# Optimization experiments

Hardware: AMD Instinct MI355X
Metric: run time of the kernel (lower is better)

The kernel has to match this reference:

```python
import jax, jax.numpy as jnp
import numpy as np

T, B, D_IN, H = 512, 64, 512, 1024


def setup_inputs() -> dict:
    key = jax.random.key(0)
    ks = jax.random.split(key, 6)
    s = 1.0 / np.sqrt(D_IN + H)  # torch Linear default init scale
    return {
        "x": jax.random.normal(ks[0], (T, B, D_IN), jnp.float32),
        "h0": jnp.zeros((B, H), jnp.float32),
        "C0": jnp.zeros((B, H), jnp.float32),
        "W_in": jax.random.normal(ks[1], (D_IN + H, H), jnp.float32) * s,
        "b_in": jnp.zeros((H,), jnp.float32),
        "W_over": jax.random.normal(ks[2], (D_IN + H, H), jnp.float32) * s,
        "b_over": jnp.zeros((H,), jnp.float32),
        "W_out": jax.random.normal(ks[3], (D_IN + H, H), jnp.float32) * s,
        "b_out": jnp.zeros((H,), jnp.float32),
        "W_intern": jax.random.normal(ks[4], (D_IN + H, H), jnp.float32) * s,
        "b_intern": jnp.zeros((H,), jnp.float32),
    }


def reference(x, h0, C0, W_in, b_in, W_over, b_over, W_out, b_out, W_intern, b_intern):
    # Faithful translation: concat order is (h, x) per one_step.
    def step(carry, xt):
        h, C = carry
        xc = jnp.concatenate([h, xt], axis=1)               # [B, H + D_IN]
        to_keep = jax.nn.sigmoid(xc @ W_in + b_in)          # input gate
        to_throw = jax.nn.sigmoid(xc @ W_over + b_over)     # forget gate
        out = jax.nn.sigmoid(xc @ W_out + b_out)            # output gate
        Ct = to_throw * C + to_keep * jnp.tanh(xc @ W_intern + b_intern)
        ht = out * jnp.tanh(Ct)
        return (ht, Ct), ht

    (hT, CT), hs = jax.lax.scan(step, (h0, C0), x)
    return hs, CT  # ([T, B, H], [B, H])
```

## Files before the change

### kernel.cpp

```cpp
#include <hip/hip_runtime.h>
#include <hip/hip_bf16.h>
#include <stdint.h>

#define T_STEPS 512
#define BATCH   64
#define DIN     512
#define HID     1024
#define KDIM    1536
#define NBLK    128
#define HPB     8
#define GCPB    32
#define KGRPS   192

typedef __bf16 bf16x8 __attribute__((ext_vector_type(8)));
typedef float  f32x4  __attribute__((ext_vector_type(4)));
typedef unsigned short ushort_t;
typedef unsigned long long u64_t;

__device__ __forceinline__ ushort_t f2bf(float f) {
    union { float f; unsigned u; } v; v.f = f;
    unsigned u = v.u;
    u += 0x7FFFu + ((u >> 16) & 1u);
    return (ushort_t)(u >> 16);
}

__device__ __forceinline__ float fast_sig(float x) {
    return __builtin_amdgcn_rcpf(1.0f + __expf(-x));
}
__device__ __forceinline__ float fast_tanh(float x) {
    float e = __expf(2.0f * x);
    return 1.0f - 2.0f * __builtin_amdgcn_rcpf(e + 1.0f);
}

__global__ void cvt_x(const float* __restrict__ x, ushort_t* __restrict__ xb, int n8) {
    int i = blockIdx.x * blockDim.x + threadIdx.x;
    if (i >= n8) return;
    float4 v0 = ((const float4*)x)[2 * i];
    float4 v1 = ((const float4*)x)[2 * i + 1];
    uint4 o;
    o.x = (unsigned)f2bf(v0.x) | ((unsigned)f2bf(v0.y) << 16);
    o.y = (unsigned)f2bf(v0.z) | ((unsigned)f2bf(v0.w) << 16);
    o.z = (unsigned)f2bf(v1.x) | ((unsigned)f2bf(v1.y) << 16);
    o.w = (unsigned)f2bf(v1.z) | ((unsigned)f2bf(v1.w) << 16);
    ((uint4*)xb)[i] = o;
}

__global__ void xpose_w(const float* __restrict__ Wi, const float* __restrict__ Wf,
                        const float* __restrict__ Wo, const float* __restrict__ Wg,
                        ushort_t* __restrict__ wt) {
    __shared__ float tile[64][65];
    int kt = blockIdx.x, nt = blockIdx.y, g = blockIdx.z;
    const float* W = (g == 0) ? Wi : (g == 1) ? Wf : (g == 2) ? Wo : Wg;
    int k0 = kt * 64, n0 = nt * 64;
    int c = threadIdx.x & 63, r0 = threadIdx.x >> 6;
#pragma unroll
    for (int i = 0; i < 16; ++i) {
        int r = r0 + i * 4;
        tile[r][c] = W[(size_t)(k0 + r) * HID + n0 + c];
    }
    __syncthreads();
#pragma unroll
    for (int p = 0; p < 2; ++p) {
        int q = threadIdx.x + p * 256;
        int n_inner = q & 7;
        int kgl = (q >> 3) & 7;
        int bl = q >> 6;
        int n = n0 + bl * 8 + n_inner;
        int blk = n >> 3;
        int nn = g * 8 + (n & 7);
        int kgrp = (k0 >> 3) + kgl;
        __align__(16) ushort_t tmp[8];
#pragma unroll
        for (int j = 0; j < 8; ++j) tmp[j] = f2bf(tile[kgl * 8 + j][bl * 8 + n_inner]);
        *(uint4*)(wt + ((((size_t)blk * KGRPS + kgrp) * GCPB + nn) << 3)) = *(const uint4*)tmp;
    }
}

__global__ __launch_bounds__(256, 1) void lstm_persist(
    const ushort_t* __restrict__ xbf,
    const ushort_t* __restrict__ wt,
    const float* __restrict__ h0, const float* __restrict__ C0,
    const float* __restrict__ b_i, const float* __restrict__ b_f,
    const float* __restrict__ b_o, const float* __restrict__ b_g,
    ushort_t* __restrict__ hbuf,
    unsigned* __restrict__ flags,
    float* __restrict__ out)
{
    __shared__ __align__(16) ushort_t Wl[KGRPS][GCPB + 1][8];
    __shared__ float gbuf[4][BATCH][GCPB + 1];
    __shared__ float Cl[BATCH][HPB + 1];
    __shared__ float biasl[GCPB];

    const int tid  = threadIdx.x;
    const int blk  = blockIdx.x;
    const int wave = tid >> 6;
    const int lane = tid & 63;
    const int j0   = blk * HPB;

    {
        const uint4* src = (const uint4*)(wt + (size_t)blk * KGRPS * GCPB * 8);
        uint4* dst = (uint4*)(&Wl[0][0][0]);
        for (int i = tid; i < 6144; i += 256) {
            int kgrp = i >> 5, n = i & 31;
            dst[kgrp * (GCPB + 1) + n] = src[i];
        }
    }
    if (tid < GCPB) {
        int g = tid >> 3, j = tid & 7;
        const float* bp = (g == 0) ? b_i : (g == 1) ? b_f : (g == 2) ? b_o : b_g;
        biasl[tid] = bp[j0 + j];
    }
    if (tid < 128) {
        int b = tid >> 1, jh = (tid & 1) * 4;
#pragma unroll
        for (int jj = 0; jj < 4; ++jj)
            Cl[b][jh + jj] = C0[b * HID + j0 + jh + jj];
        u64_t pk = 0;
#pragma unroll
        for (int jj = 0; jj < 4; ++jj)
            pk |= (u64_t)f2bf(h0[b * HID + j0 + jh + jj]) << (16 * jj);
        __hip_atomic_store((u64_t*)(hbuf + b * HID + j0 + jh), pk,
                           __ATOMIC_RELAXED, __HIP_MEMORY_SCOPE_AGENT);
    }
    asm volatile("s_waitcnt vmcnt(0)" ::: "memory");
    __syncthreads();
    if (tid == 0)
        __hip_atomic_store(&flags[blk * 32], 1u, __ATOMIC_RELAXED, __HIP_MEMORY_SCOPE_AGENT);

    const int m_lane = lane & 15;
    const int quad   = lane >> 4;
    const int koff   = quad * 8;
    int pb = 0;

    for (int t = 0; t < T_STEPS; ++t) {
        const ushort_t* hsrc = hbuf + pb * BATCH * HID;
        const ushort_t* xsrc = xbf + (size_t)t * BATCH * DIN;

        f32x4 acc[4][2];
#pragma unroll
        for (int rt = 0; rt < 4; ++rt)
#pragma unroll
            for (int ct = 0; ct < 2; ++ct)
                acc[rt][ct] = (f32x4){0.f, 0.f, 0.f, 0.f};

#pragma unroll
        for (int cc = 0; cc < 4; ++cc) {
            const int c = 32 + wave * 4 + cc;
            const ushort_t* ap = xsrc + (c - 32) * 32 + koff;
            bf16x8 a[4];
#pragma unroll
            for (int rt = 0; rt < 4; ++rt)
                a[rt] = *(const bf16x8*)(ap + (size_t)(rt * 16 + m_lane) * DIN);
            const int kgrp = c * 4 + quad;
            bf16x8 b0 = *(const bf16x8*)(&Wl[kgrp][m_lane][0]);
            bf16x8 b1 = *(const bf16x8*)(&Wl[kgrp][16 + m_lane][0]);
#pragma unroll
            for (int rt = 0; rt < 4; ++rt) {
                acc[rt][0] = __builtin_amdgcn_mfma_f32_16x16x32_bf16(a[rt], b0, acc[rt][0], 0, 0, 0);
                acc[rt][1] = __builtin_amdgcn_mfma_f32_16x16x32_bf16(a[rt], b1, acc[rt][1], 0, 0, 0);
            }
        }

        if (tid < NBLK) {
            while (__hip_atomic_load(&flags[tid * 32], __ATOMIC_RELAXED,
                                     __HIP_MEMORY_SCOPE_AGENT) < (unsigned)(t + 1))
                __builtin_amdgcn_s_sleep(1);
        }
        __syncthreads();
        __builtin_amdgcn_fence(__ATOMIC_ACQUIRE, "agent");

        bf16x8 ah[8][4];
#pragma unroll
        for (int cc = 0; cc < 8; ++cc) {
            const ushort_t* ap = hsrc + (wave * 8 + cc) * 32 + koff;
#pragma unroll
            for (int rt = 0; rt < 4; ++rt)
                ah[cc][rt] = *(const bf16x8*)(ap + (size_t)(rt * 16 + m_lane) * HID);
        }
        __builtin_amdgcn_sched_barrier(0);

#pragma unroll
        for (int cc = 0; cc < 8; ++cc) {
            const int kgrp = (wave * 8 + cc) * 4 + quad;
            bf16x8 b0 = *(const bf16x8*)(&Wl[kgrp][m_lane][0]);
            bf16x8 b1 = *(const bf16x8*)(&Wl[kgrp][16 + m_lane][0]);
#pragma unroll
            for (int rt = 0; rt < 4; ++rt) {
                acc[rt][0] = __builtin_amdgcn_mfma_f32_16x16x32_bf16(ah[cc][rt], b0, acc[rt][0], 0, 0, 0);
                acc[rt][1] = __builtin_amdgcn_mfma_f32_16x16x32_bf16(ah[cc][rt], b1, acc[rt][1], 0, 0, 0);
            }
        }

#pragma unroll
        for (int rt = 0; rt < 4; ++rt)
#pragma unroll
            for (int ct = 0; ct < 2; ++ct)
#pragma unroll
                for (int r = 0; r < 4; ++r)
                    gbuf[wave][rt * 16 + quad * 4 + r][ct * 16 + m_lane] = acc[rt][ct][r];
        __syncthreads();

        float hv[4], cv[4];
        int b = tid >> 1, jh = (tid & 1) * 4;
        if (tid < 128) {
#pragma unroll
            for (int jj = 0; jj < 4; ++jj) {
                int j = jh + jj;
                float pre[4];
#pragma unroll
                for (int g = 0; g < 4; ++g) {
                    int col = g * 8 + j;
                    pre[g] = biasl[col] + gbuf[0][b][col] + gbuf[1][b][col]
                                        + gbuf[2][b][col] + gbuf[3][b][col];
                }
                float ig = fast_sig(pre[0]);
                float fg = fast_sig(pre[1]);
                float og = fast_sig(pre[2]);
                float gg = fast_tanh(pre[3]);
                float c_new = fg * Cl[b][jh + jj] + ig * gg;
                Cl[b][jh + jj] = c_new;
                cv[jj] = c_new;
                hv[jj] = og * fast_tanh(c_new);
            }
            u64_t pk = (u64_t)f2bf(hv[0]) | ((u64_t)f2bf(hv[1]) << 16)
                     | ((u64_t)f2bf(hv[2]) << 32) | ((u64_t)f2bf(hv[3]) << 48);
            __hip_atomic_store((u64_t*)(hbuf + (1 - pb) * BATCH * HID + b * HID + j0 + jh),
                               pk, __ATOMIC_RELAXED, __HIP_MEMORY_SCOPE_AGENT);
        }
        asm volatile("s_waitcnt vmcnt(0)" ::: "memory");
        __syncthreads();
        if (tid == 0)
            __hip_atomic_store(&flags[blk * 32], (unsigned)(t + 2), __ATOMIC_RELAXED,
                               __HIP_MEMORY_SCOPE_AGENT);

        if (tid < 128) {
            float4 o4; o4.x = hv[0]; o4.y = hv[1]; o4.z = hv[2]; o4.w = hv[3];
            *(float4*)(out + (size_t)t * BATCH * HID + b * HID + j0 + jh) = o4;
            if (t == T_STEPS - 1) {
                float4 c4; c4.x = cv[0]; c4.y = cv[1]; c4.z = cv[2]; c4.w = cv[3];
                *(float4*)(out + (size_t)T_STEPS * BATCH * HID + b * HID + j0 + jh) = c4;
            }
        }
        pb ^= 1;
    }
}

extern "C" void kernel_launch(void* const* d_in, const int* in_sizes, int n_in,
                              void* d_out, int out_size, void* d_ws, size_t ws_size,
                              hipStream_t stream) {
    (void)in_sizes; (void)n_in; (void)out_size; (void)ws_size;
    const float* x  = (const float*)d_in[0];
    const float* h0 = (const float*)d_in[1];
    const float* C0 = (const float*)d_in[2];
    const float* Wi = (const float*)d_in[3];
    const float* bi = (const float*)d_in[4];
    const float* Wf = (const float*)d_in[5];
    const float* bf = (const float*)d_in[6];
    const float* Wo = (const float*)d_in[7];
    const float* bo = (const float*)d_in[8];
    const float* Wg = (const float*)d_in[9];
    const float* bg = (const float*)d_in[10];
    float* out = (float*)d_out;

    char* ws = (char*)d_ws;
    unsigned*  flags = (unsigned*)ws;
    ushort_t*  hbuf  = (ushort_t*)(ws + 16384);
    ushort_t*  xb    = (ushort_t*)(ws + 16384 + 262144);
    ushort_t*  wt    = (ushort_t*)(ws + 16384 + 262144 + 33554432);

    hipMemsetAsync(flags, 0, 16384, stream);
    cvt_x<<<8192, 256, 0, stream>>>(x, xb, (T_STEPS * BATCH * DIN) / 8);
    xpose_w<<<dim3(24, 16, 4), 256, 0, stream>>>(Wi, Wf, Wo, Wg, wt);
    lstm_persist<<<NBLK, 256, 0, stream>>>(xb, wt, h0, C0, bi, bf, bo, bg, hbuf, flags, out);
}
```

Baseline: 5.169 ms.

## Keep per-block weights in registers and defer x-projection MFMAs past barrier

Each wave now holds its slice of the weight tile (x and h parts) in VGPRs for the whole kernel instead of staging the tile in LDS and re-reading it every step. The x-input loads are issued before the inter-block flag wait, but their MFMAs now run after it, together with the h MFMAs. Empty asm statements force the loaded operands to be live before the MFMAs. This drops per-step LDS weight traffic at the cost of much higher register pressure (24 bf16x8 weight vectors plus 48 activation vectors per lane), which risks spills. The x-projection compute also moves onto the critical path after the sync instead of overlapping with the wait. The gbuf row pad changes from 33 to 34 floats.

```diff
diff --git a/kernel.cpp b/kernel.cpp
--- a/kernel.cpp
+++ b/kernel.cpp
@@ -86,8 +86,7 @@
     unsigned* __restrict__ flags,
     float* __restrict__ out)
 {
-    __shared__ __align__(16) ushort_t Wl[KGRPS][GCPB + 1][8];
-    __shared__ float gbuf[4][BATCH][GCPB + 1];
+    __shared__ float gbuf[4][BATCH][GCPB + 2];
     __shared__ float Cl[BATCH][HPB + 1];
     __shared__ float biasl[GCPB];
 
@@ -96,15 +95,25 @@
     const int wave = tid >> 6;
     const int lane = tid & 63;
     const int j0   = blk * HPB;
-
-    {
-        const uint4* src = (const uint4*)(wt + (size_t)blk * KGRPS * GCPB * 8);
-        uint4* dst = (uint4*)(&Wl[0][0][0]);
-        for (int i = tid; i < 6144; i += 256) {
-            int kgrp = i >> 5, n = i & 31;
-            dst[kgrp * (GCPB + 1) + n] = src[i];
-        }
-    }
+    const int m_lane = lane & 15;
+    const int quad   = lane >> 4;
+    const int koff   = quad * 8;
+
+    const ushort_t* wblk = wt + (size_t)blk * KGRPS * GCPB * 8;
+    bf16x8 wbx[4][2], wbh[8][2];
+#pragma unroll
+    for (int cc = 0; cc < 4; ++cc) {
+        const int kgrp = (32 + wave * 4 + cc) * 4 + quad;
+        wbx[cc][0] = *(const bf16x8*)(wblk + ((size_t)kgrp * GCPB + m_lane) * 8);
+        wbx[cc][1] = *(const bf16x8*)(wblk + ((size_t)kgrp * GCPB + 16 + m_lane) * 8);
+    }
+#pragma unroll
+    for (int cc = 0; cc < 8; ++cc) {
+        const int kgrp = (wave * 8 + cc) * 4 + quad;
+        wbh[cc][0] = *(const bf16x8*)(wblk + ((size_t)kgrp * GCPB + m_lane) * 8);
+        wbh[cc][1] = *(const bf16x8*)(wblk + ((size_t)kgrp * GCPB + 16 + m_lane) * 8);
+    }
+
     if (tid < GCPB) {
         int g = tid >> 3, j = tid & 7;
         const float* bp = (g == 0) ? b_i : (g == 1) ? b_f : (g == 2) ? b_o : b_g;
@@ -127,14 +136,10 @@
     if (tid == 0)
         __hip_atomic_store(&flags[blk * 32], 1u, __ATOMIC_RELAXED, __HIP_MEMORY_SCOPE_AGENT);
 
-    const int m_lane = lane & 15;
-    const int quad   = lane >> 4;
-    const int koff   = quad * 8;
     int pb = 0;
-
     for (int t = 0; t < T_STEPS; ++t) {
+        const ushort_t* xsrc = xbf + (size_t)t * BATCH * DIN;
         const ushort_t* hsrc = hbuf + pb * BATCH * HID;
-        const ushort_t* xsrc = xbf + (size_t)t * BATCH * DIN;
 
         f32x4 acc[4][2];
 #pragma unroll
@@ -143,23 +148,15 @@
             for (int ct = 0; ct < 2; ++ct)
                 acc[rt][ct] = (f32x4){0.f, 0.f, 0.f, 0.f};
 
+        bf16x8 ax[4][4];
 #pragma unroll
         for (int cc = 0; cc < 4; ++cc) {
-            const int c = 32 + wave * 4 + cc;
-            const ushort_t* ap = xsrc + (c - 32) * 32 + koff;
-            bf16x8 a[4];
+            const ushort_t* ap = xsrc + (wave * 4 + cc) * 32 + koff;
 #pragma unroll
             for (int rt = 0; rt < 4; ++rt)
-                a[rt] = *(const bf16x8*)(ap + (size_t)(rt * 16 + m_lane) * DIN);
-            const int kgrp = c * 4 + quad;
-            bf16x8 b0 = *(const bf16x8*)(&Wl[kgrp][m_lane][0]);
-            bf16x8 b1 = *(const bf16x8*)(&Wl[kgrp][16 + m_lane][0]);
-#pragma unroll
-            for (int rt = 0; rt < 4; ++rt) {
-                acc[rt][0] = __builtin_amdgcn_mfma_f32_16x16x32_bf16(a[rt], b0, acc[rt][0], 0, 0, 0);
-                acc[rt][1] = __builtin_amdgcn_mfma_f32_16x16x32_bf16(a[rt], b1, acc[rt][1], 0, 0, 0);
-            }
-        }
+                ax[cc][rt] = *(const bf16x8*)(ap + (size_t)(rt * 16 + m_lane) * DIN);
+        }
+        __builtin_amdgcn_sched_barrier(0);
 
         if (tid < NBLK) {
             while (__hip_atomic_load(&flags[tid * 32], __ATOMIC_RELAXED,
@@ -179,17 +176,37 @@
         }
         __builtin_amdgcn_sched_barrier(0);
 
-#pragma unroll
-        for (int cc = 0; cc < 8; ++cc) {
-            const int kgrp = (wave * 8 + cc) * 4 + quad;
-            bf16x8 b0 = *(const bf16x8*)(&Wl[kgrp][m_lane][0]);
-            bf16x8 b1 = *(const bf16x8*)(&Wl[kgrp][16 + m_lane][0]);
+        asm volatile("" ::
+            "v"(ax[0][0]), "v"(ax[0][1]), "v"(ax[0][2]), "v"(ax[0][3]),
+            "v"(ax[1][0]), "v"(ax[1][1]), "v"(ax[1][2]), "v"(ax[1][3]),
+            "v"(ax[2][0]), "v"(ax[2][1]), "v"(ax[2][2]), "v"(ax[2][3]),
+            "v"(ax[3][0]), "v"(ax[3][1]), "v"(ax[3][2]), "v"(ax[3][3]));
+#pragma unroll
+        for (int cc = 0; cc < 4; ++cc)
 #pragma unroll
             for (int rt = 0; rt < 4; ++rt) {
-                acc[rt][0] = __builtin_amdgcn_mfma_f32_16x16x32_bf16(ah[cc][rt], b0, acc[rt][0], 0, 0, 0);
-                acc[rt][1] = __builtin_amdgcn_mfma_f32_16x16x32_bf16(ah[cc][rt], b1, acc[rt][1], 0, 0, 0);
-            }
-        }
+                acc[rt][0] = __builtin_amdgcn_mfma_f32_16x16x32_bf16(ax[cc][rt], wbx[cc][0], acc[rt][0], 0, 0, 0);
+                acc[rt][1] = __builtin_amdgcn_mfma_f32_16x16x32_bf16(ax[cc][rt], wbx[cc][1], acc[rt][1], 0, 0, 0);
+            }
+
+        asm volatile("" ::
+            "v"(ah[0][0]), "v"(ah[0][1]), "v"(ah[0][2]), "v"(ah[0][3]),
+            "v"(ah[1][0]), "v"(ah[1][1]), "v"(ah[1][2]), "v"(ah[1][3]),
+            "v"(ah[2][0]), "v"(ah[2][1]), "v"(ah[2][2]), "v"(ah[2][3]),
+            "v"(ah[3][0]), "v"(ah[3][1]), "v"(ah[3][2]), "v"(ah[3][3]));
+        asm volatile("" ::
+            "v"(ah[4][0]), "v"(ah[4][1]), "v"(ah[4][2]), "v"(ah[4][3]),
+            "v"(ah[5][0]), "v"(ah[5][1]), "v"(ah[5][2]), "v"(ah[5][3]),
+            "v"(ah[6][0]), "v"(ah[6][1]), "v"(ah[6][2]), "v"(ah[6][3]),
+            "v"(ah[7][0]), "v"(ah[7][1]), "v"(ah[7][2]), "v"(ah[7][3]));
+
+#pragma unroll
+        for (int cc = 0; cc < 8; ++cc)
+#pragma unroll
+            for (int rt = 0; rt < 4; ++rt) {
+                acc[rt][0] = __builtin_amdgcn_mfma_f32_16x16x32_bf16(ah[cc][rt], wbh[cc][0], acc[rt][0], 0, 0, 0);
+                acc[rt][1] = __builtin_amdgcn_mfma_f32_16x16x32_bf16(ah[cc][rt], wbh[cc][1], acc[rt][1], 0, 0, 0);
+            }
 
 #pragma unroll
         for (int rt = 0; rt < 4; ++rt)
```

New measurement: 5.381 ms. 1.04x slower.

## Warp-specialize LSTM step: recurrent waves with register weights, input waves prefetch x

Applied to the files above, without the earlier changes.

Waves are split into two roles. Waves 0-1 keep the recurrent-weight slice in registers and do only the h·W_h product, the gate math and the h publication. Waves 2-3 keep the input-weight slice in shared memory, compute the x·W_x product, prefetch the next timestep's x, and write the fp32 outputs staged through new shared buffers. The aim is to take the x product, the x loads and the output stores off the serial dependency on the previous step's h, and to drop the recurrent-weight reads from shared memory. In exchange, each recurrent wave now does twice as many h chunks, and register pressure rises sharply.

```diff
diff --git a/kernel.cpp b/kernel.cpp
--- a/kernel.cpp
+++ b/kernel.cpp
@@ -11,6 +11,7 @@
 #define HPB     8
 #define GCPB    32
 #define KGRPS   192
+#define XKG     64
 
 typedef __bf16 bf16x8 __attribute__((ext_vector_type(8)));
 typedef float  f32x4  __attribute__((ext_vector_type(4)));
@@ -86,9 +87,11 @@
     unsigned* __restrict__ flags,
     float* __restrict__ out)
 {
-    __shared__ __align__(16) ushort_t Wl[KGRPS][GCPB + 1][8];
-    __shared__ float gbuf[4][BATCH][GCPB + 1];
+    __shared__ __align__(16) ushort_t Wlx[XKG][GCPB][8];
+    __shared__ float gbuf[4][BATCH][GCPB + 2];
     __shared__ float Cl[BATCH][HPB + 1];
+    __shared__ float hvbuf[BATCH][HPB];
+    __shared__ float cvbuf[BATCH][HPB];
     __shared__ float biasl[GCPB];
 
     const int tid  = threadIdx.x;
@@ -96,15 +99,27 @@
     const int wave = tid >> 6;
     const int lane = tid & 63;
     const int j0   = blk * HPB;
-
+    const int m_lane = lane & 15;
+    const int quad   = lane >> 4;
+    const int koff   = quad * 8;
+
+    const ushort_t* wblk = wt + (size_t)blk * KGRPS * GCPB * 8;
+
+    bf16x8 wbh[16][2];
+    if (wave < 2) {
+#pragma unroll
+        for (int cc = 0; cc < 16; ++cc) {
+            const int kgrp = (wave * 16 + cc) * 4 + quad;
+            wbh[cc][0] = *(const bf16x8*)(wblk + ((size_t)kgrp * GCPB + m_lane) * 8);
+            wbh[cc][1] = *(const bf16x8*)(wblk + ((size_t)kgrp * GCPB + 16 + m_lane) * 8);
+        }
+    }
     {
-        const uint4* src = (const uint4*)(wt + (size_t)blk * KGRPS * GCPB * 8);
-        uint4* dst = (uint4*)(&Wl[0][0][0]);
-        for (int i = tid; i < 6144; i += 256) {
-            int kgrp = i >> 5, n = i & 31;
-            dst[kgrp * (GCPB + 1) + n] = src[i];
-        }
-    }
+        const uint4* src = (const uint4*)(wblk + (size_t)128 * GCPB * 8);
+        uint4* dst = (uint4*)(&Wlx[0][0][0]);
+        for (int i = tid; i < XKG * GCPB; i += 256) dst[i] = src[i];
+    }
+
     if (tid < GCPB) {
         int g = tid >> 3, j = tid & 7;
         const float* bp = (g == 0) ? b_i : (g == 1) ? b_f : (g == 2) ? b_o : b_g;
@@ -127,82 +142,75 @@
     if (tid == 0)
         __hip_atomic_store(&flags[blk * 32], 1u, __ATOMIC_RELAXED, __HIP_MEMORY_SCOPE_AGENT);
 
-    const int m_lane = lane & 15;
-    const int quad   = lane >> 4;
-    const int koff   = quad * 8;
+    bf16x8 ax[8][4];
+    if (wave >= 2) {
+#pragma unroll
+        for (int cc = 0; cc < 8; ++cc) {
+            const ushort_t* ap = xbf + ((wave - 2) * 8 + cc) * 32 + koff;
+#pragma unroll
+            for (int rt = 0; rt < 4; ++rt)
+                ax[cc][rt] = *(const bf16x8*)(ap + (size_t)(rt * 16 + m_lane) * DIN);
+        }
+    }
+
     int pb = 0;
-
     for (int t = 0; t < T_STEPS; ++t) {
-        const ushort_t* hsrc = hbuf + pb * BATCH * HID;
-        const ushort_t* xsrc = xbf + (size_t)t * BATCH * DIN;
-
-        f32x4 acc[4][2];
-#pragma unroll
-        for (int rt = 0; rt < 4; ++rt)
-#pragma unroll
-            for (int ct = 0; ct < 2; ++ct)
-                acc[rt][ct] = (f32x4){0.f, 0.f, 0.f, 0.f};
-
-#pragma unroll
-        for (int cc = 0; cc < 4; ++cc) {
-            const int c = 32 + wave * 4 + cc;
-            const ushort_t* ap = xsrc + (c - 32) * 32 + koff;
-            bf16x8 a[4];
-#pragma unroll
-            for (int rt = 0; rt < 4; ++rt)
-                a[rt] = *(const bf16x8*)(ap + (size_t)(rt * 16 + m_lane) * DIN);
-            const int kgrp = c * 4 + quad;
-            bf16x8 b0 = *(const bf16x8*)(&Wl[kgrp][m_lane][0]);
-            bf16x8 b1 = *(const bf16x8*)(&Wl[kgrp][16 + m_lane][0]);
-#pragma unroll
-            for (int rt = 0; rt < 4; ++rt) {
-                acc[rt][0] = __builtin_amdgcn_mfma_f32_16x16x32_bf16(a[rt], b0, acc[rt][0], 0, 0, 0);
-                acc[rt][1] = __builtin_amdgcn_mfma_f32_16x16x32_bf16(a[rt], b1, acc[rt][1], 0, 0, 0);
-            }
-        }
-
-        if (tid < NBLK) {
+        if (wave < 2) {
             while (__hip_atomic_load(&flags[tid * 32], __ATOMIC_RELAXED,
                                      __HIP_MEMORY_SCOPE_AGENT) < (unsigned)(t + 1))
                 __builtin_amdgcn_s_sleep(1);
-        }
-        __syncthreads();
-        __builtin_amdgcn_fence(__ATOMIC_ACQUIRE, "agent");
-
-        bf16x8 ah[8][4];
-#pragma unroll
-        for (int cc = 0; cc < 8; ++cc) {
-            const ushort_t* ap = hsrc + (wave * 8 + cc) * 32 + koff;
+            __syncthreads();
+            __builtin_amdgcn_fence(__ATOMIC_ACQUIRE, "agent");
+            __builtin_amdgcn_sched_barrier(0);
+
+            const ushort_t* hsrc = hbuf + pb * BATCH * HID;
+            const int hc0 = wave * 16;
+
+            f32x4 acc[4][2];
+#pragma unroll
+            for (int rt = 0; rt < 4; ++rt) {
+                acc[rt][0] = (f32x4){0.f, 0.f, 0.f, 0.f};
+                acc[rt][1] = (f32x4){0.f, 0.f, 0.f, 0.f};
+            }
+
+            bf16x8 a0[4][4], a1[4][4], a2[4][4], a3[4][4];
+#define LOADB(dst, c0)                                                        \
+            _Pragma("unroll") for (int q = 0; q < 4; ++q) {                   \
+                const ushort_t* ap = hsrc + (size_t)(hc0 + (c0) + q) * 32 + koff; \
+                _Pragma("unroll") for (int rt = 0; rt < 4; ++rt)              \
+                    dst[q][rt] = *(const bf16x8*)(ap + (size_t)(rt * 16 + m_lane) * HID); \
+            }
+#define MFMAB(src, c0)                                                        \
+            _Pragma("unroll") for (int q = 0; q < 4; ++q) {                   \
+                _Pragma("unroll") for (int rt = 0; rt < 4; ++rt) {            \
+                    acc[rt][0] = __builtin_amdgcn_mfma_f32_16x16x32_bf16(     \
+                        src[q][rt], wbh[(c0) + q][0], acc[rt][0], 0, 0, 0);   \
+                    acc[rt][1] = __builtin_amdgcn_mfma_f32_16x16x32_bf16(     \
+                        src[q][rt], wbh[(c0) + q][1], acc[rt][1], 0, 0, 0);   \
+                }                                                             \
+            }
+            LOADB(a0, 0)
+            LOADB(a1, 4)
+            MFMAB(a0, 0)
+            LOADB(a2, 8)
+            MFMAB(a1, 4)
+            LOADB(a3, 12)
+            MFMAB(a2, 8)
+            MFMAB(a3, 12)
+#undef LOADB
+#undef MFMAB
+
 #pragma unroll
             for (int rt = 0; rt < 4; ++rt)
-                ah[cc][rt] = *(const bf16x8*)(ap + (size_t)(rt * 16 + m_lane) * HID);
-        }
-        __builtin_amdgcn_sched_barrier(0);
-
-#pragma unroll
-        for (int cc = 0; cc < 8; ++cc) {
-            const int kgrp = (wave * 8 + cc) * 4 + quad;
-            bf16x8 b0 = *(const bf16x8*)(&Wl[kgrp][m_lane][0]);
-            bf16x8 b1 = *(const bf16x8*)(&Wl[kgrp][16 + m_lane][0]);
-#pragma unroll
-            for (int rt = 0; rt < 4; ++rt) {
-                acc[rt][0] = __builtin_amdgcn_mfma_f32_16x16x32_bf16(ah[cc][rt], b0, acc[rt][0], 0, 0, 0);
-                acc[rt][1] = __builtin_amdgcn_mfma_f32_16x16x32_bf16(ah[cc][rt], b1, acc[rt][1], 0, 0, 0);
-            }
-        }
-
-#pragma unroll
-        for (int rt = 0; rt < 4; ++rt)
-#pragma unroll
-            for (int ct = 0; ct < 2; ++ct)
-#pragma unroll
-                for (int r = 0; r < 4; ++r)
-                    gbuf[wave][rt * 16 + quad * 4 + r][ct * 16 + m_lane] = acc[rt][ct][r];
-        __syncthreads();
-
-        float hv[4], cv[4];
-        int b = tid >> 1, jh = (tid & 1) * 4;
-        if (tid < 128) {
+#pragma unroll
+                for (int ct = 0; ct < 2; ++ct)
+#pragma unroll
+                    for (int r = 0; r < 4; ++r)
+                        gbuf[wave][rt * 16 + quad * 4 + r][ct * 16 + m_lane] = acc[rt][ct][r];
+            __syncthreads();
+
+            float hv[4], cv[4];
+            const int b = tid >> 1, jh = (tid & 1) * 4;
 #pragma unroll
             for (int jj = 0; jj < 4; ++jj) {
                 int j = jh + jj;
@@ -222,22 +230,69 @@
                 cv[jj] = c_new;
                 hv[jj] = og * fast_tanh(c_new);
             }
+            {
+                float4 o4; o4.x = hv[0]; o4.y = hv[1]; o4.z = hv[2]; o4.w = hv[3];
+                *(float4*)(&hvbuf[b][jh]) = o4;
+                if (t == T_STEPS - 1) {
+                    float4 c4; c4.x = cv[0]; c4.y = cv[1]; c4.z = cv[2]; c4.w = cv[3];
+                    *(float4*)(&cvbuf[b][jh]) = c4;
+                }
+            }
             u64_t pk = (u64_t)f2bf(hv[0]) | ((u64_t)f2bf(hv[1]) << 16)
                      | ((u64_t)f2bf(hv[2]) << 32) | ((u64_t)f2bf(hv[3]) << 48);
             __hip_atomic_store((u64_t*)(hbuf + (1 - pb) * BATCH * HID + b * HID + j0 + jh),
                                pk, __ATOMIC_RELAXED, __HIP_MEMORY_SCOPE_AGENT);
-        }
-        asm volatile("s_waitcnt vmcnt(0)" ::: "memory");
-        __syncthreads();
-        if (tid == 0)
-            __hip_atomic_store(&flags[blk * 32], (unsigned)(t + 2), __ATOMIC_RELAXED,
-                               __HIP_MEMORY_SCOPE_AGENT);
-
-        if (tid < 128) {
-            float4 o4; o4.x = hv[0]; o4.y = hv[1]; o4.z = hv[2]; o4.w = hv[3];
+            asm volatile("s_waitcnt vmcnt(0)" ::: "memory");
+            __syncthreads();
+            if (tid == 0)
+                __hip_atomic_store(&flags[blk * 32], (unsigned)(t + 2), __ATOMIC_RELAXED,
+                                   __HIP_MEMORY_SCOPE_AGENT);
+        } else {
+            f32x4 acc[4][2];
+#pragma unroll
+            for (int rt = 0; rt < 4; ++rt) {
+                acc[rt][0] = (f32x4){0.f, 0.f, 0.f, 0.f};
+                acc[rt][1] = (f32x4){0.f, 0.f, 0.f, 0.f};
+            }
+#pragma unroll
+            for (int cc = 0; cc < 8; ++cc) {
+                const int kgx = ((wave - 2) * 8 + cc) * 4 + quad;
+                bf16x8 b0 = *(const bf16x8*)(&Wlx[kgx][m_lane][0]);
+                bf16x8 b1 = *(const bf16x8*)(&Wlx[kgx][16 + m_lane][0]);
+#pragma unroll
+                for (int rt = 0; rt < 4; ++rt) {
+                    acc[rt][0] = __builtin_amdgcn_mfma_f32_16x16x32_bf16(ax[cc][rt], b0, acc[rt][0], 0, 0, 0);
+                    acc[rt][1] = __builtin_amdgcn_mfma_f32_16x16x32_bf16(ax[cc][rt], b1, acc[rt][1], 0, 0, 0);
+                }
+            }
+#pragma unroll
+            for (int rt = 0; rt < 4; ++rt)
+#pragma unroll
+                for (int ct = 0; ct < 2; ++ct)
+#pragma unroll
+                    for (int r = 0; r < 4; ++r)
+                        gbuf[wave][rt * 16 + quad * 4 + r][ct * 16 + m_lane] = acc[rt][ct][r];
+            __syncthreads();
+
+            if (t + 1 < T_STEPS) {
+                const ushort_t* xsrc = xbf + (size_t)(t + 1) * BATCH * DIN;
+#pragma unroll
+                for (int cc = 0; cc < 8; ++cc) {
+                    const ushort_t* ap = xsrc + ((wave - 2) * 8 + cc) * 32 + koff;
+#pragma unroll
+                    for (int rt = 0; rt < 4; ++rt)
+                        ax[cc][rt] = *(const bf16x8*)(ap + (size_t)(rt * 16 + m_lane) * DIN);
+                }
+            }
+            __syncthreads();
+            __syncthreads();
+
+            const int tid2 = tid - 128;
+            const int b = tid2 >> 1, jh = (tid2 & 1) * 4;
+            float4 o4 = *(const float4*)(&hvbuf[b][jh]);
             *(float4*)(out + (size_t)t * BATCH * HID + b * HID + j0 + jh) = o4;
             if (t == T_STEPS - 1) {
-                float4 c4; c4.x = cv[0]; c4.y = cv[1]; c4.z = cv[2]; c4.w = cv[3];
+                float4 c4 = *(const float4*)(&cvbuf[b][jh]);
                 *(float4*)(out + (size_t)T_STEPS * BATCH * HID + b * HID + j0 + jh) = c4;
             }
         }
```

Result: slower. 6.037 ms (+16.8%).
